# Kernel optimization log

Measured on AMD Instinct MI355X. Metric: run time of the kernel, lower is better.

The kernel has to match this reference:

```python
import jax, jax.numpy as jnp
import numpy as np

TIME_STEP = 32
BATCH = 1048576


def setup_inputs() -> dict:
    key = jax.random.key(0)
    k_x, k_w, k_b = jax.random.split(key, 3)
    inputs = jax.random.normal(k_x, (BATCH, TIME_STEP), dtype=jnp.float32)
    # Row t of W holds the weights of nn.Linear(t+1, 1); entries j>t are unused (masked).
    # Match torch Linear init scale: U(-1/sqrt(fan_in), 1/sqrt(fan_in)) per row, roughly -> just use small uniform.
    W = jax.random.uniform(k_w, (TIME_STEP, TIME_STEP), dtype=jnp.float32, minval=-0.5, maxval=0.5)
    b = jax.random.uniform(k_b, (TIME_STEP,), dtype=jnp.float32, minval=-0.5, maxval=0.5)
    return {"inputs": inputs, "W": W, "b": b}


def reference(inputs, W, b):
    # out[n, t] = sum_{j <= t} W[t, j] * inputs[n, j] + b[t]
    # Fuse the T tiny linears into one triangular-masked matmul.
    Wtri = jnp.tril(W)                       # [T, T] lower triangular
    return jnp.einsum("nj,tj->nt", inputs, Wtri) + b  # [B, T]
```

## Files before the change

### kernel.cpp

```cpp
#include <hip/hip_runtime.h>


constexpr int T    = 32;
constexpr int ROWS = 256;
constexpr int RSTR = T + 1;

__global__ __launch_bounds__(256) void triu_kernel(
    const float* __restrict__ x, const float* __restrict__ W,
    const float* __restrict__ b, float* __restrict__ out)
{
    __shared__ float sX[ROWS * RSTR];

    const int tid = threadIdx.x;
    const long long base = (long long)blockIdx.x * (ROWS * T);

    const float4* __restrict__ x4 = reinterpret_cast<const float4*>(x + base);
    #pragma unroll
    for (int it = 0; it < (ROWS * T) / (256 * 4); ++it) {
        const int idx = it * 256 + tid;
        const float4 v = x4[idx];
        const int row = idx >> 3;
        const int col = (idx & 7) << 2;
        const int p = row * RSTR + col;
        sX[p + 0] = v.x; sX[p + 1] = v.y; sX[p + 2] = v.z; sX[p + 3] = v.w;
    }
    __syncthreads();

    float* myrow = &sX[tid * RSTR];
    float xr[T];
    #pragma unroll
    for (int j = 0; j < T; ++j) xr[j] = myrow[j];

    #pragma unroll
    for (int t = 0; t < T; ++t) {
        float acc = b[t];
        #pragma unroll
        for (int j = 0; j <= t; ++j)
            acc = fmaf(W[t * T + j], xr[j], acc);
        myrow[t] = acc;
    }
    __syncthreads();

    float4* __restrict__ o4 = reinterpret_cast<float4*>(out + base);
    #pragma unroll
    for (int it = 0; it < 8; ++it) {
        const int idx = it * 256 + tid;
        const int row = idx >> 3;
        const int col = (idx & 7) << 2;
        const int p = row * RSTR + col;
        o4[idx] = make_float4(sX[p + 0], sX[p + 1], sX[p + 2], sX[p + 3]);
    }
}

extern "C" void kernel_launch(void* const* d_in, const int* in_sizes, int n_in,
                              void* d_out, int out_size, void* d_ws, size_t ws_size,
                              hipStream_t stream) {
    const float* x  = (const float*)d_in[0];
    const float* W  = (const float*)d_in[1];
    const float* b  = (const float*)d_in[2];
    float* out      = (float*)d_out;

    const int batch = in_sizes[0] / T;
    const int grid  = batch / ROWS;
    triu_kernel<<<grid, 256, 0, stream>>>(x, W, b, out);
}
```

Before: 240.6 us.

## Load input directly into LDS and use XOR-swizzled float4 shared layout

Replaces the register-staged global-to-shared copy with global_load_lds direct-to-LDS loads, and changes the shared buffer from a padded scalar layout to an XOR-swizzled float4 layout. Per-thread row reads and writes and the coalesced output pass become 128-bit LDS accesses, while the swizzle is meant to avoid bank conflicts. The aim is to cut VGPR staging and the many scalar LDS instructions. The cost is reliance on the 16-byte global_load_lds builtin being supported on this target, plus holding all 32 outputs in registers before writing them back.

```diff
diff --git a/kernel.cpp b/kernel.cpp
--- a/kernel.cpp
+++ b/kernel.cpp
@@ -3,52 +3,63 @@
 
 constexpr int T    = 32;
 constexpr int ROWS = 256;
-constexpr int RSTR = T + 1;
 
 __global__ __launch_bounds__(256) void triu_kernel(
     const float* __restrict__ x, const float* __restrict__ W,
     const float* __restrict__ b, float* __restrict__ out)
 {
-    __shared__ float sX[ROWS * RSTR];
+    __shared__ float4 sX[ROWS * 8];
 
-    const int tid = threadIdx.x;
-    const long long base = (long long)blockIdx.x * (ROWS * T);
+    const int tid  = threadIdx.x;
+    const int lane = tid & 63;
+    const int wid  = tid >> 6;
+    const long long base4 = (long long)blockIdx.x * (ROWS * 8);
 
-    const float4* __restrict__ x4 = reinterpret_cast<const float4*>(x + base);
+    const float4* __restrict__ x4 = reinterpret_cast<const float4*>(x) + base4;
+
     #pragma unroll
-    for (int it = 0; it < (ROWS * T) / (256 * 4); ++it) {
-        const int idx = it * 256 + tid;
-        const float4 v = x4[idx];
-        const int row = idx >> 3;
-        const int col = (idx & 7) << 2;
-        const int p = row * RSTR + col;
-        sX[p + 0] = v.x; sX[p + 1] = v.y; sX[p + 2] = v.z; sX[p + 3] = v.w;
+    for (int it = 0; it < 8; ++it) {
+        const int s   = it * 256 + wid * 64 + lane;
+        const int row = s >> 3;
+        const int c   = (s & 7) ^ (row & 7);
+        __builtin_amdgcn_global_load_lds(
+            (const __attribute__((address_space(1))) void*)(x4 + row * 8 + c),
+            (__attribute__((address_space(3))) void*)(&sX[it * 256 + wid * 64]),
+            16, 0, 0);
     }
     __syncthreads();
 
-    float* myrow = &sX[tid * RSTR];
+    const int r7 = tid & 7;
     float xr[T];
     #pragma unroll
-    for (int j = 0; j < T; ++j) xr[j] = myrow[j];
+    for (int k = 0; k < 8; ++k) {
+        const float4 v = sX[tid * 8 + (k ^ r7)];
+        xr[4 * k + 0] = v.x; xr[4 * k + 1] = v.y;
+        xr[4 * k + 2] = v.z; xr[4 * k + 3] = v.w;
+    }
+
+    float acc[T];
+    #pragma unroll
+    for (int t = 0; t < T; ++t) {
+        float a = b[t];
+        #pragma unroll
+        for (int j = 0; j <= t; ++j)
+            a = fmaf(W[t * T + j], xr[j], a);
+        acc[t] = a;
+    }
 
     #pragma unroll
-    for (int t = 0; t < T; ++t) {
-        float acc = b[t];
-        #pragma unroll
-        for (int j = 0; j <= t; ++j)
-            acc = fmaf(W[t * T + j], xr[j], acc);
-        myrow[t] = acc;
-    }
+    for (int k = 0; k < 8; ++k)
+        sX[tid * 8 + (k ^ r7)] = make_float4(acc[4 * k + 0], acc[4 * k + 1],
+                                             acc[4 * k + 2], acc[4 * k + 3]);
     __syncthreads();
 
-    float4* __restrict__ o4 = reinterpret_cast<float4*>(out + base);
+    float4* __restrict__ o4 = reinterpret_cast<float4*>(out) + base4;
     #pragma unroll
     for (int it = 0; it < 8; ++it) {
         const int idx = it * 256 + tid;
         const int row = idx >> 3;
-        const int col = (idx & 7) << 2;
-        const int p = row * RSTR + col;
-        o4[idx] = make_float4(sX[p + 0], sX[p + 1], sX[p + 2], sX[p + 3]);
+        o4[idx] = sX[row * 8 + ((idx & 7) ^ (row & 7))];
     }
 }
 
```

After: 243.5 us. Within noise of the previous version (+1.2%).
